# Optimization experiments

Hardware: AMD Instinct MI355X
Metric: run time of the kernel (lower is better)

Reference implementation:

```python
import jax, jax.numpy as jnp
import numpy as np

TEMPERATURE = 0.1
EPS = 1e-12  # F.normalize eps

B, D = 4096, 1024

def setup_inputs() -> dict:
    key = jax.random.key(0)
    k1, k2 = jax.random.split(key)
    return {
        "feature_view_1": jax.random.normal(k1, (B, D), dtype=jnp.float32),
        "feature_view_2": jax.random.normal(k2, (B, D), dtype=jnp.float32),
    }

def reference(feature_view_1, feature_view_2):
    b = feature_view_1.shape[0]
    n = 2 * b  # n_views = 2
    # cat views and L2-normalize each row (F.normalize semantics: x / max(||x||, eps))
    f = jnp.concatenate([feature_view_1, feature_view_2], axis=0)  # [2B, D]
    norm = jnp.maximum(jnp.linalg.norm(f, axis=1, keepdims=True), EPS)
    f = f / norm
    # similarity matrix scaled by temperature
    sim = jnp.matmul(f, f.T) / TEMPERATURE  # [2B, 2B]
    idx = jnp.arange(n)
    # positive for row i is the other view of the same sample: column (i+B) mod 2B
    pos = sim[idx, (idx + b) % n]  # [2B]
    # cross-entropy with label 0 over [pos, negatives] == lse over off-diagonal minus pos
    sim_offdiag = jnp.where(idx[:, None] == idx[None, :], -jnp.inf, sim)
    lse = jax.nn.logsumexp(sim_offdiag, axis=1)  # [2B]
    # CrossEntropyLoss default reduction: mean
    return jnp.mean(lse - pos)
```

## Files before the change

kernel.cpp:

```cpp
#include <hip/hip_runtime.h>
#include <stdint.h>

#define B_ROWS 4096
#define N_ROWS 8192
#define D_DIM  1024
#define NBLK   64
#define NTRI   2080
#define XCDQ   260

typedef __attribute__((ext_vector_type(4))) float f32x4;
typedef __attribute__((ext_vector_type(2))) long longx2;

static __device__ __forceinline__ void async_copy16(const unsigned char* g, unsigned char* l) {
  __builtin_amdgcn_global_load_lds(
      (const __attribute__((address_space(1))) unsigned int*)g,
      (__attribute__((address_space(3))) unsigned int*)l, 16, 0, 0);
}

static __device__ __forceinline__ void wg_barrier() {
  asm volatile("" ::: "memory");
  __builtin_amdgcn_s_barrier();
  asm volatile("" ::: "memory");
}

__global__ __launch_bounds__(256) void normalize_kernel(
    const float* __restrict__ f1, const float* __restrict__ f2,
    unsigned char* __restrict__ F8, float* __restrict__ rowsum) {
  const int row = blockIdx.x;
  const int tid = threadIdx.x;
  const float* src = (row < B_ROWS) ? (f1 + (size_t)row * D_DIM)
                                    : (f2 + (size_t)(row - B_ROWS) * D_DIM);
  float4 v = ((const float4*)src)[tid];
  float ss = v.x * v.x + v.y * v.y + v.z * v.z + v.w * v.w;
#pragma unroll
  for (int m = 1; m < 64; m <<= 1) ss += __shfl_xor(ss, m, 64);
  __shared__ float red[4];
  if ((tid & 63) == 0) red[tid >> 6] = ss;
  __syncthreads();
  ss = red[0] + red[1] + red[2] + red[3];
  const float s16 = 16.0f / fmaxf(sqrtf(ss), 1e-12f);
  int w = 0;
  w = __builtin_amdgcn_cvt_pk_fp8_f32(v.x * s16, v.y * s16, w, 0);
  w = __builtin_amdgcn_cvt_pk_fp8_f32(v.z * s16, v.w * s16, w, 1);
  const int idx = (tid >> 4) * 16 + ((tid >> 1) & 3) * 4 +
                  ((tid >> 3) & 1) * 2 + (tid & 1);
  ((int*)(F8 + (size_t)row * D_DIM))[idx] = w;
  if (tid == 0) rowsum[row] = 0.0f;
}

__global__ __launch_bounds__(256, 3) void simloss_kernel(
    const unsigned char* __restrict__ F8, float* __restrict__ rowsum,
    float* __restrict__ pos) {
  __shared__ __align__(16) unsigned char lA[3][128 * 64];
  __shared__ __align__(16) unsigned char lB[3][128 * 64];

  int s = (blockIdx.x & 7) * XCDQ + (blockIdx.x >> 3);
  int SJ = 0;
  for (;;) { const int c = 64 * SJ + 36; if (s < c) break; s -= c; ++SJ; }
  int SI = 0;
  while (SI < SJ && s >= 64) { s -= 64; ++SI; }
  int di, dj;
  if (SI < SJ) {
    dj = s >> 3; di = s & 7;
  } else {
    dj = 0; while (s > dj) { s -= (dj + 1); ++dj; } di = s;
  }
  const int bi = SI * 8 + di;
  const int bj = SJ * 8 + dj;

  const int tid  = threadIdx.x;
  const int lane = tid & 63;
  const int wv   = __builtin_amdgcn_readfirstlane(tid >> 6);
  const int waveRow = wv >> 1;
  const int waveCol = wv & 1;
  const int q   = lane >> 4;
  const int l16 = lane & 15;

  const int iBase = bi * 128;
  const int jBase = bj * 128;
  const unsigned char* __restrict__ GA = F8 + (size_t)iBase * D_DIM;
  const unsigned char* __restrict__ GB = F8 + (size_t)jBase * D_DIM;

  f32x4 acc[4][4];
#pragma unroll
  for (int a = 0; a < 4; ++a)
#pragma unroll
    for (int b = 0; b < 4; ++b) acc[a][b] = (f32x4){0.f, 0.f, 0.f, 0.f};

#define STAGE(BUFI, K0)                                                      \
  {                                                                          \
    _Pragma("unroll") for (int it = 0; it < 2; ++it) {                       \
      const int lc = it * 256 + tid;                                         \
      const int rr = lc >> 2;                                                \
      const int gc = (lc & 3) ^ ((rr >> 1) & 3);                             \
      const size_t goff = (size_t)rr * D_DIM + (K0) + gc * 16;               \
      async_copy16(GA + goff, &lA[BUFI][lc * 16]);                           \
    }                                                                        \
    _Pragma("unroll") for (int it = 0; it < 2; ++it) {                       \
      const int lc = it * 256 + tid;                                         \
      const int rr = lc >> 2;                                                \
      const int gc = (lc & 3) ^ ((rr >> 1) & 3);                             \
      const size_t goff = (size_t)rr * D_DIM + (K0) + gc * 16;               \
      async_copy16(GB + goff, &lB[BUFI][lc * 16]);                           \
    }                                                                        \
  }

#define STEP(BUFI)                                                           \
  {                                                                          \
    longx2 aF[4], bF[4];                                                     \
    _Pragma("unroll") for (int mi = 0; mi < 4; ++mi) {                       \
      const int rr = waveRow * 64 + mi * 16 + l16;                           \
      const int ch = rr * 4 + (q ^ ((rr >> 1) & 3));                         \
      aF[mi] = *(const longx2*)&lA[BUFI][ch * 16];                           \
    }                                                                        \
    _Pragma("unroll") for (int ni = 0; ni < 4; ++ni) {                       \
      const int rr = waveCol * 64 + ni * 16 + l16;                           \
      const int ch = rr * 4 + (q ^ ((rr >> 1) & 3));                         \
      bF[ni] = *(const longx2*)&lB[BUFI][ch * 16];                           \
    }                                                                        \
    _Pragma("unroll") for (int mi = 0; mi < 4; ++mi)                         \
      _Pragma("unroll") for (int ni = 0; ni < 4; ++ni) {                     \
        acc[mi][ni] = __builtin_amdgcn_mfma_f32_16x16x32_fp8_fp8(            \
            aF[mi].x, bF[ni].x, acc[mi][ni], 0, 0, 0);                       \
        acc[mi][ni] = __builtin_amdgcn_mfma_f32_16x16x32_fp8_fp8(            \
            aF[mi].y, bF[ni].y, acc[mi][ni], 0, 0, 0);                       \
      }                                                                      \
  }

  STAGE(0, 0)
  STAGE(1, 64)

#pragma unroll 1
  for (int t = 0; t < 16; ++t) {
    if (t == 15) { asm volatile("s_waitcnt vmcnt(0)" ::: "memory"); }
    else         { asm volatile("s_waitcnt vmcnt(4)" ::: "memory"); }
    wg_barrier();
    if (t < 14) { STAGE((t + 2) % 3, (t + 2) * 64) }
    STEP(t % 3)
  }
#undef STEP
#undef STAGE

  const bool offdiag = (bi != bj);
  float colAcc[4] = {0.f, 0.f, 0.f, 0.f};

#pragma unroll
  for (int mi = 0; mi < 4; ++mi) {
#pragma unroll
    for (int reg = 0; reg < 4; ++reg) {
      const int i = iBase + waveRow * 64 + mi * 16 + q * 4 + reg;
      float s2 = 0.0f;
#pragma unroll
      for (int ni = 0; ni < 4; ++ni) {
        const int j = jBase + waveCol * 64 + ni * 16 + l16;
        const float sim = acc[mi][ni][reg] * (10.0f / 256.0f);
        const float e = (j == i) ? 0.0f : __expf(sim - 10.0f);
        s2 += e;
        colAcc[ni] += e;
        if (i < B_ROWS && j == i + B_ROWS) pos[i] = sim;
      }
#pragma unroll
      for (int m = 1; m < 16; m <<= 1) s2 += __shfl_xor(s2, m, 64);
      if (l16 == 0) atomicAdd(&rowsum[i], s2);
    }
  }

  if (offdiag) {
#pragma unroll
    for (int ni = 0; ni < 4; ++ni) {
      float c = colAcc[ni];
      c += __shfl_xor(c, 16, 64);
      c += __shfl_xor(c, 32, 64);
      if (q == 0) {
        const int j = jBase + waveCol * 64 + ni * 16 + l16;
        atomicAdd(&rowsum[j], c);
      }
    }
  }
}

__global__ __launch_bounds__(1024) void finalize_kernel(
    const float* __restrict__ rowsum, const float* __restrict__ pos,
    float* __restrict__ out) {
  const int tid = threadIdx.x;
  float a = 0.0f;
  for (int i = tid; i < N_ROWS; i += 1024)
    a += logf(rowsum[i]) + 10.0f - pos[i & (B_ROWS - 1)];
#pragma unroll
  for (int m = 1; m < 64; m <<= 1) a += __shfl_xor(a, m, 64);
  __shared__ float red[16];
  if ((tid & 63) == 0) red[tid >> 6] = a;
  __syncthreads();
  if (tid == 0) {
    float t = 0.0f;
#pragma unroll
    for (int w = 0; w < 16; ++w) t += red[w];
    out[0] = t * (1.0f / N_ROWS);
  }
}

extern "C" void kernel_launch(void* const* d_in, const int* in_sizes, int n_in,
                              void* d_out, int out_size, void* d_ws, size_t ws_size,
                              hipStream_t stream) {
  const float* f1 = (const float*)d_in[0];
  const float* f2 = (const float*)d_in[1];
  unsigned char* F8 = (unsigned char*)d_ws;
  float* rowsum = (float*)((char*)d_ws + (size_t)N_ROWS * D_DIM);
  float* pos    = rowsum + N_ROWS;
  float* out    = (float*)d_out;

  hipLaunchKernelGGL(normalize_kernel, dim3(N_ROWS), dim3(256), 0, stream, f1, f2, F8, rowsum);
  hipLaunchKernelGGL(simloss_kernel, dim3(NTRI), dim3(256), 0, stream, F8, rowsum, pos);
  hipLaunchKernelGGL(finalize_kernel, dim3(1), dim3(1024), 0, stream, rowsum, pos, out);
}
```

Before: 144.9 us.

## Fuse finalize reduction into simloss via per-row-block completion counters

Drops the single-block finalize kernel. Each tile now bumps per-row-block counters, and the last tile to finish a 128-row block computes that block's log-sum terms and adds them to a global accumulator. The positive-pair terms are also accumulated atomically instead of being stored to a separate array. This removes one kernel launch and the serial tail. In exchange it adds atomic contention, extra barriers in every tile, and relies on memory ordering between the rowsum atomics and the counter increment, so the output may be nondeterministic.

```diff
diff --git a/kernel.cpp b/kernel.cpp
--- a/kernel.cpp
+++ b/kernel.cpp
@@ -25,7 +25,8 @@
 
 __global__ __launch_bounds__(256) void normalize_kernel(
     const float* __restrict__ f1, const float* __restrict__ f2,
-    unsigned char* __restrict__ F8, float* __restrict__ rowsum) {
+    unsigned char* __restrict__ F8, float* __restrict__ rowsum,
+    int* __restrict__ cnt ) {
   const int row = blockIdx.x;
   const int tid = threadIdx.x;
   const float* src = (row < B_ROWS) ? (f1 + (size_t)row * D_DIM)
@@ -46,13 +47,19 @@
                   ((tid >> 3) & 1) * 2 + (tid & 1);
   ((int*)(F8 + (size_t)row * D_DIM))[idx] = w;
   if (tid == 0) rowsum[row] = 0.0f;
+  if (row == 0 && tid < 66) cnt[tid] = 0;
 }
 
 __global__ __launch_bounds__(256, 3) void simloss_kernel(
     const unsigned char* __restrict__ F8, float* __restrict__ rowsum,
-    float* __restrict__ pos) {
+    int* __restrict__ cnt, float* __restrict__ out) {
   __shared__ __align__(16) unsigned char lA[3][128 * 64];
   __shared__ __align__(16) unsigned char lB[3][128 * 64];
+  __shared__ int finrb[2];
+  __shared__ float redf[4];
+
+  int* fin = cnt + 64;
+  float* acc_g = (float*)(cnt + 65);
 
   int s = (blockIdx.x & 7) * XCDQ + (blockIdx.x >> 3);
   int SJ = 0;
@@ -143,6 +150,7 @@
 
   const bool offdiag = (bi != bj);
   float colAcc[4] = {0.f, 0.f, 0.f, 0.f};
+  float posAcc = 0.0f;
 
 #pragma unroll
   for (int mi = 0; mi < 4; ++mi) {
@@ -157,7 +165,7 @@
         const float e = (j == i) ? 0.0f : __expf(sim - 10.0f);
         s2 += e;
         colAcc[ni] += e;
-        if (i < B_ROWS && j == i + B_ROWS) pos[i] = sim;
+        if (i < B_ROWS && j == i + B_ROWS) posAcc -= 2.0f * sim;
       }
 #pragma unroll
       for (int m = 1; m < 16; m <<= 1) s2 += __shfl_xor(s2, m, 64);
@@ -177,25 +185,44 @@
       }
     }
   }
-}
-
-__global__ __launch_bounds__(1024) void finalize_kernel(
-    const float* __restrict__ rowsum, const float* __restrict__ pos,
-    float* __restrict__ out) {
-  const int tid = threadIdx.x;
-  float a = 0.0f;
-  for (int i = tid; i < N_ROWS; i += 1024)
-    a += logf(rowsum[i]) + 10.0f - pos[i & (B_ROWS - 1)];
-#pragma unroll
-  for (int m = 1; m < 64; m <<= 1) a += __shfl_xor(a, m, 64);
-  __shared__ float red[16];
-  if ((tid & 63) == 0) red[tid >> 6] = a;
+
+#pragma unroll
+  for (int m = 1; m < 64; m <<= 1) posAcc += __shfl_xor(posAcc, m, 64);
+  if (lane == 0 && posAcc != 0.0f) atomicAdd(acc_g, posAcc);
+
   __syncthreads();
   if (tid == 0) {
-    float t = 0.0f;
-#pragma unroll
-    for (int w = 0; w < 16; ++w) t += red[w];
-    out[0] = t * (1.0f / N_ROWS);
+    finrb[0] = (atomicAdd(&cnt[bi], 1) == 63) ? bi : -1;
+    finrb[1] = (offdiag && atomicAdd(&cnt[bj], 1) == 63) ? bj : -1;
+  }
+  __syncthreads();
+
+#pragma unroll
+  for (int f = 0; f < 2; ++f) {
+    const int rb = finrb[f];
+    if (rb >= 0) {
+      float a = 0.0f;
+      if (tid < 128) {
+        const float rs = __hip_atomic_load(&rowsum[rb * 128 + tid],
+                                           __ATOMIC_RELAXED,
+                                           __HIP_MEMORY_SCOPE_AGENT);
+        a = __logf(rs) + 10.0f;
+      }
+#pragma unroll
+      for (int m = 1; m < 64; m <<= 1) a += __shfl_xor(a, m, 64);
+      if (lane == 0) redf[wv] = a;
+      __syncthreads();
+      if (tid == 0) {
+        atomicAdd(acc_g, redf[0] + redf[1] + redf[2] + redf[3]);
+        asm volatile("s_waitcnt vmcnt(0)" ::: "memory");
+        if (atomicAdd(fin, 1) == 63) {
+          const float res = __hip_atomic_load(acc_g, __ATOMIC_RELAXED,
+                                              __HIP_MEMORY_SCOPE_AGENT);
+          out[0] = res * (1.0f / N_ROWS);
+        }
+      }
+      __syncthreads();
+    }
   }
 }
 
@@ -206,10 +233,11 @@
   const float* f2 = (const float*)d_in[1];
   unsigned char* F8 = (unsigned char*)d_ws;
   float* rowsum = (float*)((char*)d_ws + (size_t)N_ROWS * D_DIM);
-  float* pos    = rowsum + N_ROWS;
+  int*   cnt    = (int*)(rowsum + N_ROWS);
   float* out    = (float*)d_out;
 
-  hipLaunchKernelGGL(normalize_kernel, dim3(N_ROWS), dim3(256), 0, stream, f1, f2, F8, rowsum);
-  hipLaunchKernelGGL(simloss_kernel, dim3(NTRI), dim3(256), 0, stream, F8, rowsum, pos);
-  hipLaunchKernelGGL(finalize_kernel, dim3(1), dim3(1024), 0, stream, rowsum, pos, out);
-}
+  hipLaunchKernelGGL(normalize_kernel, dim3(N_ROWS), dim3(256), 0, stream,
+                     f1, f2, F8, rowsum, cnt);
+  hipLaunchKernelGGL(simloss_kernel, dim3(NTRI), dim3(256), 0, stream,
+                     F8, rowsum, cnt, out);
+}
```

Measured after the change: 149.3 us. 3.0% more time.
